# Kernel tuning notes

Measured on AMD Instinct MI355X. Metric: run time of the kernel, lower is better.

## Reference

```python
import jax, jax.numpy as jnp
import numpy as np

B, S, D = 8, 2048, 1024
E, K = 16, 2
H = 4096
SD, SH = D // E, H // E  # 64, 256
MAX_SEQ = 2048


def setup_inputs() -> dict:
    key = jax.random.key(0)
    ks = jax.random.split(key, 5)
    x = jax.random.normal(ks[0], (B, S, D), dtype=jnp.float32)
    w_switch = jax.random.normal(ks[1], (D * MAX_SEQ, E), dtype=jnp.float32) * 0.001
    b_switch = jnp.zeros((E,), dtype=jnp.float32)
    w1 = jax.random.normal(ks[2], (E, SD, SH), dtype=jnp.float32) * (1.0 / np.sqrt(SD))
    b1 = jnp.zeros((E, SH), dtype=jnp.float32)
    w2 = jax.random.normal(ks[3], (H, D), dtype=jnp.float32) * (1.0 / np.sqrt(H))
    b2 = jnp.zeros((D,), dtype=jnp.float32)
    return {"x": x, "w_switch": w_switch, "b_switch": b_switch,
            "w1": w1, "b1": b1, "w2": w2, "b2": b2}


def reference(x, w_switch, b_switch, w1, b1, w2, b2):
    # Router: softmax over experts from flattened first MAX_SEQ tokens
    x0 = x[:, :MAX_SEQ].reshape(B, -1)                      # [B, D*MAX_SEQ]
    route_prob = jax.nn.softmax(x0 @ w_switch + b_switch)   # [B, E]
    # Top-k expert membership mask per batch element
    _, topk_idx = jax.lax.top_k(route_prob, K)              # [B, K]
    mask = jax.nn.one_hot(topk_idx, E, dtype=x.dtype).sum(axis=1)  # [B, E]
    # Per-expert linear on the expert's channel slice, masked combine
    xe = x.reshape(B, S, E, SD)                              # [B, S, E, SD]
    h = jnp.einsum('bsed,edh->bseh', xe, w1) + b1            # [B, S, E, SH]
    h = h * mask[:, None, :, None]                           # zero out non-routed
    out = h.reshape(B, S, H)                                 # [B, S, H]
    out = jax.nn.gelu(out, approximate=False)                # exact GELU (torch default)
    return out @ w2 + b2                                     # [B, S, D]
```

## Files before the change

kernel.cpp:

```cpp
#include <hip/hip_runtime.h>
#include <hip/hip_bf16.h>

#define B_  8
#define S_  2048
#define D_  1024
#define E_  16
#define SD_ 64
#define SH_ 256
#define H_  4096
#define R_  (D_ * S_)
#define NBLK_ 8192

typedef __attribute__((ext_vector_type(8))) short bf16x8;
typedef __attribute__((ext_vector_type(4))) float f32x4;

static __device__ __forceinline__ short f2bf(float f) {
    union { float f; unsigned u; } v; v.f = f;
    unsigned r = v.u + 0x7fffu + ((v.u >> 16) & 1u);
    return (short)(r >> 16);
}

__global__ void convert_w(const float* __restrict__ w1, const float* __restrict__ w2,
                          short* __restrict__ w1f, short* __restrict__ w2f) {
    int blk = blockIdx.x;
    if (blk < 128) {
        int t = blk * 256 + threadIdx.x;
        int lane = t & 63, ntile = (t >> 6) & 15, ks = (t >> 10) & 1, e = t >> 11;
        int k0 = ks * 32 + ((lane >> 4) << 3);
        int n  = (ntile << 4) + (lane & 15);
        const float* src = w1 + ((size_t)(e * 64 + k0) * 256 + n);
        bf16x8 o;
        #pragma unroll
        for (int j = 0; j < 8; ++j) o[j] = f2bf(src[(size_t)j * 256]);
        *(bf16x8*)(w1f + ((size_t)t << 3)) = o;
    } else {
        int t = (blk - 128) * 256 + threadIdx.x;
        int lane = t & 63, ntile = (t >> 6) & 63, kg = t >> 12;
        int k0 = (kg << 5) + ((lane >> 4) << 3);
        int n  = (ntile << 4) + (lane & 15);
        const float* src = w2 + ((size_t)k0 * 1024 + n);
        bf16x8 o;
        #pragma unroll
        for (int j = 0; j < 8; ++j) o[j] = f2bf(src[(size_t)j * 1024]);
        *(bf16x8*)(w2f + ((size_t)t << 3)) = o;
    }
}

__global__ __launch_bounds__(256, 4) void router_kernel(const float* __restrict__ x,
                                                        const float* __restrict__ wsw,
                                                        float* __restrict__ partials) {
    __shared__ float red[512];
    int tid = threadIdx.x;
    int wid = tid >> 6, lane = tid & 63;
    int q = lane & 3, rsub = lane >> 2;
    size_t wavebase = (((size_t)blockIdx.x << 2) + wid) << 6;
    const float4* wp = (const float4*)wsw + (wavebase << 2) + lane;

    float4 w0 = wp[0];
    float4 w1 = wp[64];
    float4 w2 = wp[128];
    float4 w3 = wp[192];
    float xv[4][8];
    #pragma unroll
    for (int b = 0; b < 8; ++b) {
        const float* xb = x + (size_t)b * R_ + wavebase + rsub;
        #pragma unroll
        for (int it = 0; it < 4; ++it)
            xv[it][b] = xb[it << 4];
    }

    float acc[8][4];
    #pragma unroll
    for (int b = 0; b < 8; ++b)
        #pragma unroll
        for (int j = 0; j < 4; ++j) acc[b][j] = 0.f;

    #define FMA4(W, IT)                                             \
        _Pragma("unroll")                                           \
        for (int b = 0; b < 8; ++b) {                               \
            float xs = xv[IT][b];                                   \
            acc[b][0] = fmaf(xs, (W).x, acc[b][0]);                 \
            acc[b][1] = fmaf(xs, (W).y, acc[b][1]);                 \
            acc[b][2] = fmaf(xs, (W).z, acc[b][2]);                 \
            acc[b][3] = fmaf(xs, (W).w, acc[b][3]);                 \
        }
    FMA4(w0, 0)
    FMA4(w1, 1)
    FMA4(w2, 2)
    FMA4(w3, 3)
    #undef FMA4

    #pragma unroll
    for (int b = 0; b < 8; ++b)
        #pragma unroll
        for (int j = 0; j < 4; ++j) {
            float v = acc[b][j];
            v += __shfl_xor(v, 4);
            v += __shfl_xor(v, 8);
            v += __shfl_xor(v, 16);
            v += __shfl_xor(v, 32);
            acc[b][j] = v;
        }

    if (lane < 4) {
        #pragma unroll
        for (int b = 0; b < 8; ++b)
            #pragma unroll
            for (int j = 0; j < 4; ++j)
                red[(wid << 7) + b * 16 + q * 4 + j] = acc[b][j];
    }
    __syncthreads();
    if (tid < 128)
        partials[(size_t)tid * NBLK_ + blockIdx.x] =
            red[tid] + red[128 + tid] + red[256 + tid] + red[384 + tid];
}

__global__ __launch_bounds__(256) void reduce_kernel(const float* __restrict__ partials,
                                                     float* __restrict__ logits) {
    __shared__ float s[256];
    int e = blockIdx.x, tid = threadIdx.x;
    const float4* p4 = (const float4*)(partials + (size_t)e * NBLK_);
    float t = 0.f;
    #pragma unroll
    for (int i = 0; i < 8; ++i) {
        float4 v = p4[i * 256 + tid];
        t += v.x + v.y + v.z + v.w;
    }
    s[tid] = t;
    __syncthreads();
    #pragma unroll
    for (int off = 128; off; off >>= 1) {
        if (tid < off) s[tid] += s[tid + off];
        __syncthreads();
    }
    if (tid == 0) logits[e] = s[0];
}

__global__ void topk_kernel(const float* __restrict__ logits,
                            const float* __restrict__ bsw,
                            int* __restrict__ experts) {
    int b = threadIdx.x;
    if (b >= 8) return;
    float v[16];
    #pragma unroll
    for (int e = 0; e < 16; ++e) v[e] = logits[b * 16 + e] + bsw[e];
    int i0 = 0; float m0 = v[0];
    #pragma unroll
    for (int e = 1; e < 16; ++e) if (v[e] > m0) { m0 = v[e]; i0 = e; }
    int i1 = -1; float m1 = -3.4e38f;
    #pragma unroll
    for (int e = 0; e < 16; ++e) if (e != i0 && v[e] > m1) { m1 = v[e]; i1 = e; }
    experts[2 * b]     = i0;
    experts[2 * b + 1] = i1;
}

__global__ __launch_bounds__(256, 2) void mlp_kernel(
        const float* __restrict__ x, const int* __restrict__ experts,
        const short* __restrict__ w1f, const float* __restrict__ b1,
        const short* __restrict__ w2f, const float* __restrict__ b2,
        float* __restrict__ out) {
    __shared__ short G[32][520];

    int blk  = blockIdx.x;
    int b    = blk & 7;
    int tok0 = (blk >> 3) << 5;
    int e0 = experts[2 * b], e1 = experts[2 * b + 1];
    int tid = threadIdx.x;
    int wid = tid >> 6, lane = tid & 63;
    int slot  = wid >> 1;
    int ex    = slot ? e1 : e0;
    int nhalf = wid & 1;
    int lrow = lane & 15, lk8 = (lane >> 4) << 3;

    f32x4 acc1[2][8];
    #pragma unroll
    for (int m = 0; m < 2; ++m)
        #pragma unroll
        for (int n = 0; n < 8; ++n) acc1[m][n] = (f32x4){0.f, 0.f, 0.f, 0.f};

    #pragma unroll
    for (int ks = 0; ks < 2; ++ks) {
        bf16x8 a[2];
        #pragma unroll
        for (int m = 0; m < 2; ++m) {
            const float* xp = x + (((size_t)b * S_ + tok0 + m * 16 + lrow) * D_
                                   + ex * 64 + ks * 32 + lk8);
            float4 f0 = *(const float4*)xp;
            float4 f1 = *(const float4*)(xp + 4);
            bf16x8 av;
            av[0] = f2bf(f0.x); av[1] = f2bf(f0.y); av[2] = f2bf(f0.z); av[3] = f2bf(f0.w);
            av[4] = f2bf(f1.x); av[5] = f2bf(f1.y); av[6] = f2bf(f1.z); av[7] = f2bf(f1.w);
            a[m] = av;
        }
        #pragma unroll
        for (int nt = 0; nt < 8; ++nt) {
            int ntg = nhalf * 8 + nt;
            bf16x8 bf = *(const bf16x8*)(w1f + ((((size_t)(ex * 2 + ks) * 16 + ntg) * 64 + lane) << 3));
            acc1[0][nt] = __builtin_amdgcn_mfma_f32_16x16x32_bf16(a[0], bf, acc1[0][nt], 0, 0, 0);
            acc1[1][nt] = __builtin_amdgcn_mfma_f32_16x16x32_bf16(a[1], bf, acc1[1][nt], 0, 0, 0);
        }
    }

    #pragma unroll
    for (int nt = 0; nt < 8; ++nt) {
        int ncol = (nhalf * 8 + nt) * 16 + lrow;
        float bb = b1[ex * 256 + ncol];
        #pragma unroll
        for (int m = 0; m < 2; ++m) {
            int r0 = m * 16 + ((lane >> 4) << 2);
            #pragma unroll
            for (int r = 0; r < 4; ++r) {
                float v = acc1[m][nt][r] + bb;
                v = 0.5f * v * (1.0f + erff(v * 0.70710678118f));
                G[r0 + r][slot * 256 + ncol] = f2bf(v);
            }
        }
    }
    __syncthreads();

    f32x4 acc2[2][16];
    #pragma unroll
    for (int m = 0; m < 2; ++m)
        #pragma unroll
        for (int n = 0; n < 16; ++n) acc2[m][n] = (f32x4){0.f, 0.f, 0.f, 0.f};

    for (int ks = 0; ks < 16; ++ks) {
        int e  = (ks < 8) ? e0 : e1;
        int kg = e * 8 + (ks & 7);
        bf16x8 a0 = *(const bf16x8*)&G[lrow][ks * 32 + lk8];
        bf16x8 a1 = *(const bf16x8*)&G[16 + lrow][ks * 32 + lk8];
        #pragma unroll
        for (int nt = 0; nt < 16; ++nt) {
            int ntg = wid * 16 + nt;
            bf16x8 bf = *(const bf16x8*)(w2f + ((((size_t)kg * 64 + ntg) * 64 + lane) << 3));
            acc2[0][nt] = __builtin_amdgcn_mfma_f32_16x16x32_bf16(a0, bf, acc2[0][nt], 0, 0, 0);
            acc2[1][nt] = __builtin_amdgcn_mfma_f32_16x16x32_bf16(a1, bf, acc2[1][nt], 0, 0, 0);
        }
    }

    size_t obase = ((size_t)b * S_ + tok0) * D_;
    #pragma unroll
    for (int nt = 0; nt < 16; ++nt) {
        int d = wid * 256 + nt * 16 + lrow;
        float bb = b2[d];
        #pragma unroll
        for (int m = 0; m < 2; ++m) {
            int r0 = m * 16 + ((lane >> 4) << 2);
            #pragma unroll
            for (int r = 0; r < 4; ++r)
                out[obase + (size_t)(r0 + r) * D_ + d] = acc2[m][nt][r] + bb;
        }
    }
}

extern "C" void kernel_launch(void* const* d_in, const int* in_sizes, int n_in,
                              void* d_out, int out_size, void* d_ws, size_t ws_size,
                              hipStream_t stream) {
    const float* x   = (const float*)d_in[0];
    const float* wsw = (const float*)d_in[1];
    const float* bsw = (const float*)d_in[2];
    const float* w1  = (const float*)d_in[3];
    const float* b1  = (const float*)d_in[4];
    const float* w2  = (const float*)d_in[5];
    const float* b2  = (const float*)d_in[6];
    float* out = (float*)d_out;

    int*   experts  = (int*)d_ws;
    float* logits   = (float*)((char*)d_ws + 512);
    float* partials = (float*)((char*)d_ws + 4096);
    short* w1f = (short*)((char*)d_ws + 4096 + 4194304);
    short* w2f = (short*)((char*)d_ws + 4096 + 4194304 + 524288);

    router_kernel<<<NBLK_, 256, 0, stream>>>(x, wsw, partials);
    reduce_kernel<<<128, 256, 0, stream>>>(partials, logits);
    topk_kernel<<<1, 64, 0, stream>>>(logits, bsw, experts);
    convert_w<<<2176, 256, 0, stream>>>(w1, w2, w1f, w2f);
    mlp_kernel<<<512, 256, 0, stream>>>(x, experts, w1f, b1, w2f, b2, out);
}
```

Before: 128.0 us.

## Halve MLP token tile to 16 rows and transpose router partials layout

The MLP kernel now processes 16 tokens per block instead of 32 and launches 1024 blocks. This halves accumulator registers, so the launch bound is raised to 3 blocks per SIMD for more occupancy. The cost is that each w2 fragment is reused across fewer rows, roughly doubling weight traffic per token. Router partials are now written contiguously per block, with the reduce kernel reading strided instead, and the weight conversion launch is moved ahead of the reduce and top-k launches.

Result: slower. 163.4 us (+27.7%).

```diff
diff --git a/kernel.cpp b/kernel.cpp
--- a/kernel.cpp
+++ b/kernel.cpp
@@ -54,12 +54,12 @@
     int wid = tid >> 6, lane = tid & 63;
     int q = lane & 3, rsub = lane >> 2;
     size_t wavebase = (((size_t)blockIdx.x << 2) + wid) << 6;
-    const float4* wp = (const float4*)wsw + (wavebase << 2) + lane;
-
-    float4 w0 = wp[0];
-    float4 w1 = wp[64];
-    float4 w2 = wp[128];
-    float4 w3 = wp[192];
+    const f32x4* wp = (const f32x4*)wsw + (wavebase << 2) + lane;
+
+    f32x4 w0 = wp[0];
+    f32x4 w1v = wp[64];
+    f32x4 w2v = wp[128];
+    f32x4 w3v = wp[192];
     float xv[4][8];
     #pragma unroll
     for (int b = 0; b < 8; ++b) {
@@ -79,15 +79,15 @@
         _Pragma("unroll")                                           \
         for (int b = 0; b < 8; ++b) {                               \
             float xs = xv[IT][b];                                   \
-            acc[b][0] = fmaf(xs, (W).x, acc[b][0]);                 \
-            acc[b][1] = fmaf(xs, (W).y, acc[b][1]);                 \
-            acc[b][2] = fmaf(xs, (W).z, acc[b][2]);                 \
-            acc[b][3] = fmaf(xs, (W).w, acc[b][3]);                 \
+            acc[b][0] = fmaf(xs, (W)[0], acc[b][0]);                \
+            acc[b][1] = fmaf(xs, (W)[1], acc[b][1]);                \
+            acc[b][2] = fmaf(xs, (W)[2], acc[b][2]);                \
+            acc[b][3] = fmaf(xs, (W)[3], acc[b][3]);                \
         }
     FMA4(w0, 0)
-    FMA4(w1, 1)
-    FMA4(w2, 2)
-    FMA4(w3, 3)
+    FMA4(w1v, 1)
+    FMA4(w2v, 2)
+    FMA4(w3v, 3)
     #undef FMA4
 
     #pragma unroll
@@ -111,7 +111,7 @@
     }
     __syncthreads();
     if (tid < 128)
-        partials[(size_t)tid * NBLK_ + blockIdx.x] =
+        partials[(size_t)blockIdx.x * 128 + tid] =
             red[tid] + red[128 + tid] + red[256 + tid] + red[384 + tid];
 }
 
@@ -119,13 +119,10 @@
                                                      float* __restrict__ logits) {
     __shared__ float s[256];
     int e = blockIdx.x, tid = threadIdx.x;
-    const float4* p4 = (const float4*)(partials + (size_t)e * NBLK_);
     float t = 0.f;
     #pragma unroll
-    for (int i = 0; i < 8; ++i) {
-        float4 v = p4[i * 256 + tid];
-        t += v.x + v.y + v.z + v.w;
-    }
+    for (int k = 0; k < 32; ++k)
+        t += partials[(size_t)(tid + (k << 8)) * 128 + e];
     s[tid] = t;
     __syncthreads();
     #pragma unroll
@@ -154,16 +151,16 @@
     experts[2 * b + 1] = i1;
 }
 
-__global__ __launch_bounds__(256, 2) void mlp_kernel(
+__global__ __launch_bounds__(256, 3) void mlp_kernel(
         const float* __restrict__ x, const int* __restrict__ experts,
         const short* __restrict__ w1f, const float* __restrict__ b1,
         const short* __restrict__ w2f, const float* __restrict__ b2,
         float* __restrict__ out) {
-    __shared__ short G[32][520];
+    __shared__ short G[16][520];
 
     int blk  = blockIdx.x;
     int b    = blk & 7;
-    int tok0 = (blk >> 3) << 5;
+    int tok0 = (blk >> 3) << 4;
     int e0 = experts[2 * b], e1 = experts[2 * b + 1];
     int tid = threadIdx.x;
     int wid = tid >> 6, lane = tid & 63;
@@ -171,33 +168,26 @@
     int ex    = slot ? e1 : e0;
     int nhalf = wid & 1;
     int lrow = lane & 15, lk8 = (lane >> 4) << 3;
-
-    f32x4 acc1[2][8];
-    #pragma unroll
-    for (int m = 0; m < 2; ++m)
-        #pragma unroll
-        for (int n = 0; n < 8; ++n) acc1[m][n] = (f32x4){0.f, 0.f, 0.f, 0.f};
+    int r0 = (lane >> 4) << 2;
+
+    f32x4 acc1[8];
+    #pragma unroll
+    for (int n = 0; n < 8; ++n) acc1[n] = (f32x4){0.f, 0.f, 0.f, 0.f};
 
     #pragma unroll
     for (int ks = 0; ks < 2; ++ks) {
-        bf16x8 a[2];
-        #pragma unroll
-        for (int m = 0; m < 2; ++m) {
-            const float* xp = x + (((size_t)b * S_ + tok0 + m * 16 + lrow) * D_
-                                   + ex * 64 + ks * 32 + lk8);
-            float4 f0 = *(const float4*)xp;
-            float4 f1 = *(const float4*)(xp + 4);
-            bf16x8 av;
-            av[0] = f2bf(f0.x); av[1] = f2bf(f0.y); av[2] = f2bf(f0.z); av[3] = f2bf(f0.w);
-            av[4] = f2bf(f1.x); av[5] = f2bf(f1.y); av[6] = f2bf(f1.z); av[7] = f2bf(f1.w);
-            a[m] = av;
-        }
+        const float* xp = x + (((size_t)b * S_ + tok0 + lrow) * D_
+                               + ex * 64 + ks * 32 + lk8);
+        float4 f0 = *(const float4*)xp;
+        float4 f1 = *(const float4*)(xp + 4);
+        bf16x8 a;
+        a[0] = f2bf(f0.x); a[1] = f2bf(f0.y); a[2] = f2bf(f0.z); a[3] = f2bf(f0.w);
+        a[4] = f2bf(f1.x); a[5] = f2bf(f1.y); a[6] = f2bf(f1.z); a[7] = f2bf(f1.w);
         #pragma unroll
         for (int nt = 0; nt < 8; ++nt) {
             int ntg = nhalf * 8 + nt;
             bf16x8 bf = *(const bf16x8*)(w1f + ((((size_t)(ex * 2 + ks) * 16 + ntg) * 64 + lane) << 3));
-            acc1[0][nt] = __builtin_amdgcn_mfma_f32_16x16x32_bf16(a[0], bf, acc1[0][nt], 0, 0, 0);
-            acc1[1][nt] = __builtin_amdgcn_mfma_f32_16x16x32_bf16(a[1], bf, acc1[1][nt], 0, 0, 0);
+            acc1[nt] = __builtin_amdgcn_mfma_f32_16x16x32_bf16(a, bf, acc1[nt], 0, 0, 0);
         }
     }
 
@@ -206,35 +196,27 @@
         int ncol = (nhalf * 8 + nt) * 16 + lrow;
         float bb = b1[ex * 256 + ncol];
         #pragma unroll
-        for (int m = 0; m < 2; ++m) {
-            int r0 = m * 16 + ((lane >> 4) << 2);
-            #pragma unroll
-            for (int r = 0; r < 4; ++r) {
-                float v = acc1[m][nt][r] + bb;
-                v = 0.5f * v * (1.0f + erff(v * 0.70710678118f));
-                G[r0 + r][slot * 256 + ncol] = f2bf(v);
-            }
+        for (int r = 0; r < 4; ++r) {
+            float v = acc1[nt][r] + bb;
+            v = 0.5f * v * (1.0f + erff(v * 0.70710678118f));
+            G[r0 + r][slot * 256 + ncol] = f2bf(v);
         }
     }
     __syncthreads();
 
-    f32x4 acc2[2][16];
-    #pragma unroll
-    for (int m = 0; m < 2; ++m)
-        #pragma unroll
-        for (int n = 0; n < 16; ++n) acc2[m][n] = (f32x4){0.f, 0.f, 0.f, 0.f};
+    f32x4 acc2[16];
+    #pragma unroll
+    for (int n = 0; n < 16; ++n) acc2[n] = (f32x4){0.f, 0.f, 0.f, 0.f};
 
     for (int ks = 0; ks < 16; ++ks) {
         int e  = (ks < 8) ? e0 : e1;
         int kg = e * 8 + (ks & 7);
         bf16x8 a0 = *(const bf16x8*)&G[lrow][ks * 32 + lk8];
-        bf16x8 a1 = *(const bf16x8*)&G[16 + lrow][ks * 32 + lk8];
         #pragma unroll
         for (int nt = 0; nt < 16; ++nt) {
             int ntg = wid * 16 + nt;
             bf16x8 bf = *(const bf16x8*)(w2f + ((((size_t)kg * 64 + ntg) * 64 + lane) << 3));
-            acc2[0][nt] = __builtin_amdgcn_mfma_f32_16x16x32_bf16(a0, bf, acc2[0][nt], 0, 0, 0);
-            acc2[1][nt] = __builtin_amdgcn_mfma_f32_16x16x32_bf16(a1, bf, acc2[1][nt], 0, 0, 0);
+            acc2[nt] = __builtin_amdgcn_mfma_f32_16x16x32_bf16(a0, bf, acc2[nt], 0, 0, 0);
         }
     }
 
@@ -244,12 +226,8 @@
         int d = wid * 256 + nt * 16 + lrow;
         float bb = b2[d];
         #pragma unroll
-        for (int m = 0; m < 2; ++m) {
-            int r0 = m * 16 + ((lane >> 4) << 2);
-            #pragma unroll
-            for (int r = 0; r < 4; ++r)
-                out[obase + (size_t)(r0 + r) * D_ + d] = acc2[m][nt][r] + bb;
-        }
+        for (int r = 0; r < 4; ++r)
+            out[obase + (size_t)(r0 + r) * D_ + d] = acc2[nt][r] + bb;
     }
 }
 
@@ -272,8 +250,8 @@
     short* w2f = (short*)((char*)d_ws + 4096 + 4194304 + 524288);
 
     router_kernel<<<NBLK_, 256, 0, stream>>>(x, wsw, partials);
+    convert_w<<<2176, 256, 0, stream>>>(w1, w2, w1f, w2f);
     reduce_kernel<<<128, 256, 0, stream>>>(partials, logits);
     topk_kernel<<<1, 64, 0, stream>>>(logits, bsw, experts);
-    convert_w<<<2176, 256, 0, stream>>>(w1, w2, w1f, w2f);
-    mlp_kernel<<<512, 256, 0, stream>>>(x, experts, w1f, b1, w2f, b2, out);
-}
+    mlp_kernel<<<1024, 256, 0, stream>>>(x, experts, w1f, b1, w2f, b2, out);
+}
```
